# Performance work log

Hardware: AMD Instinct MI355X
Metric: run time of the kernel (lower is better)

The kernel has to match this reference:

```python
import jax, jax.numpy as jnp
import numpy as np

N = 100_000      # nodes
E = 1_600_000    # edges (avg degree 16)
FIN = 128
FOUT = 64
C = 1.0          # Poincare ball curvature (args.c)
T = 0.48         # threshold (forward default)
MIN_NORM = 1e-15
PROJ_EPS = 4e-3  # float32 boundary eps used by standard PoincareBall.proj


def _artanh(x):
    x = jnp.clip(x, -1.0 + 1e-7, 1.0 - 1e-7)
    return 0.5 * (jnp.log1p(x) - jnp.log1p(-x))


def logmap0(p, c):
    sc = c ** 0.5
    n = jnp.clip(jnp.linalg.norm(p, axis=-1, keepdims=True), MIN_NORM, None)
    return p / (sc * n) * _artanh(sc * n)


def expmap0(u, c):
    sc = c ** 0.5
    n = jnp.clip(jnp.linalg.norm(u, axis=-1, keepdims=True), MIN_NORM, None)
    return jnp.tanh(sc * n) * u / (sc * n)


def proj(x, c):
    n = jnp.clip(jnp.linalg.norm(x, axis=-1, keepdims=True), MIN_NORM, None)
    maxn = (1.0 - PROJ_EPS) / (c ** 0.5)
    return jnp.where(n > maxn, x / n * maxn, x)


def setup_inputs() -> dict:
    key = jax.random.key(0)
    k0, k1, k2, k3, k4 = jax.random.split(key, 5)
    # points near the origin of the Poincare ball
    x = jax.random.normal(k0, (N, FIN), dtype=jnp.float32) * 0.05
    edge_index = jax.random.randint(k1, (2, E), 0, N, dtype=jnp.int32)
    W_up = jax.random.normal(k2, (FIN, FOUT), dtype=jnp.float32) / np.float32(np.sqrt(FIN))
    W_pl = jax.random.normal(k3, (FOUT, 2), dtype=jnp.float32) / np.float32(np.sqrt(FOUT))
    W_lw = jax.random.normal(k4, (2 * FOUT, 1), dtype=jnp.float32) / np.float32(np.sqrt(2 * FOUT))
    return {"x": x, "edge_index": edge_index, "W_up": W_up, "W_pl": W_pl, "W_lw": W_lw}


def reference(x, edge_index, W_up, W_pl, W_lw):
    src, dst = edge_index[0], edge_index[1]

    def agg(v):  # PyG add-aggregation: out[i] = sum_{(j->i)} v[j]
        return jax.ops.segment_sum(v[src], dst, num_segments=N)

    x_tan = logmap0(x, C)                                   # [N, FIN]
    updated_x = jax.nn.leaky_relu(x_tan @ W_up)             # [N, FOUT], slope 0.01
    sum_neigh = agg(updated_x)                              # [N, FOUT]
    random_prob = jax.nn.softmax(jax.nn.relu(sum_neigh @ W_pl), axis=-1)  # [N, 2]
    sel_v = jnp.where(random_prob[:, 1:2] > T, 1.0, 0.0)    # [N, 1] hard gate
    sum_sel = agg(sel_v * updated_x)                        # [N, FOUT]
    weight_sel = jax.nn.sigmoid(jnp.concatenate([sum_sel, sum_neigh], axis=-1) @ W_lw)  # [N, 1]
    a_x = jax.nn.relu(agg(weight_sel * sel_v * updated_x))  # [N, FOUT]
    out = updated_x + a_x
    return proj(expmap0(out, C), C)
```

## Files before the change

kernel.cpp:

```cpp
#include <hip/hip_runtime.h>
#include <math.h>

#define FIN 128
#define FOUT 64
#define MAXDEG 64
#define BKT_SHIFT 7
#define BKT_CAP 2560


__device__ __forceinline__ float4 f4add(float4 a, float4 b) {
  return make_float4(a.x + b.x, a.y + b.y, a.z + b.z, a.w + b.w);
}
__device__ __forceinline__ float4 f4fma(float c, float4 v, float4 a) {
  return make_float4(fmaf(c, v.x, a.x), fmaf(c, v.y, a.y),
                     fmaf(c, v.z, a.z), fmaf(c, v.w, a.w));
}
__device__ __forceinline__ float4 f4shflxor(float4 v, int off) {
  return make_float4(__shfl_xor(v.x, off, 64), __shfl_xor(v.y, off, 64),
                     __shfl_xor(v.z, off, 64), __shfl_xor(v.w, off, 64));
}
__device__ __forceinline__ float red16(float v) {
  v += __shfl_xor(v, 1, 64);
  v += __shfl_xor(v, 2, 64);
  v += __shfl_xor(v, 4, 64);
  v += __shfl_xor(v, 8, 64);
  return v;
}

__device__ __forceinline__ float row_scale(float ss) {
  float n  = sqrtf(ss);
  float nc = fmaxf(n, 1e-15f);
  float t  = fminf(nc, 1.0f - 1e-7f);
  float at = 0.5f * (log1pf(t) - log1pf(-t));
  return at / nc;
}

__device__ __forceinline__ float leaky(float v) {
  return (v >= 0.f) ? v : 0.01f * v;
}

__device__ __forceinline__ unsigned int bf16rne(float x) {
  unsigned int b = __float_as_uint(x);
  b += 0x7FFFu + ((b >> 16) & 1u);
  return b >> 16;
}
__device__ __forceinline__ float4 bf4(uint2 v) {
  return make_float4(__uint_as_float(v.x << 16),
                     __uint_as_float(v.x & 0xFFFF0000u),
                     __uint_as_float(v.y << 16),
                     __uint_as_float(v.y & 0xFFFF0000u));
}

__global__ __launch_bounds__(256) void k_main(const float* __restrict__ x,
                                              const float* __restrict__ Wup,
                                              const float* __restrict__ Wpl,
                                              const float* __restrict__ Wlw,
                                              float* __restrict__ u,
                                              float* __restrict__ scl4,
                                              const int* __restrict__ ei, int E,
                                              int nb, int* __restrict__ bcnt,
                                              int2* __restrict__ stg,
                                              int N, int gemmBlocks) {
  __shared__ float buf[8192];
  __shared__ float wls[256];
  __shared__ float ps[256];
  __shared__ float scl[64];

  int t = threadIdx.x;

  if (blockIdx.x >= gemmBlocks) {
    int* hist = (int*)buf;
    int* base = hist + nb;
    int bb = blockIdx.x - gemmBlocks;
    for (int h = t; h < nb; h += 256) hist[h] = 0;
    __syncthreads();
    int e0 = bb * 4096 + t * 16;
    int sv[16], dv[16];
#pragma unroll
    for (int j = 0; j < 16; j += 4) {
      int e = e0 + j;
      if (e + 3 < E) {
        int4 s4 = *(const int4*)(ei + e);
        int4 d4 = *(const int4*)(ei + E + e);
        sv[j] = s4.x; sv[j+1] = s4.y; sv[j+2] = s4.z; sv[j+3] = s4.w;
        dv[j] = d4.x; dv[j+1] = d4.y; dv[j+2] = d4.z; dv[j+3] = d4.w;
      } else {
        for (int q = 0; q < 4; ++q) {
          int ee = e + q;
          sv[j+q] = (ee < E) ? ei[ee] : -1;
          dv[j+q] = (ee < E) ? ei[E + ee] : -1;
        }
      }
    }
#pragma unroll
    for (int j = 0; j < 16; ++j)
      if (dv[j] >= 0) atomicAdd(&hist[dv[j] >> BKT_SHIFT], 1);
    __syncthreads();
    for (int h = t; h < nb; h += 256)
      base[h] = hist[h] ? atomicAdd(&bcnt[h], hist[h]) : 0;
    __syncthreads();
    for (int h = t; h < nb; h += 256) hist[h] = 0;
    __syncthreads();
#pragma unroll
    for (int j = 0; j < 16; ++j) {
      if (dv[j] < 0) continue;
      int b = dv[j] >> BKT_SHIFT;
      int p = base[b] + atomicAdd(&hist[b], 1);
      if (p < BKT_CAP) stg[(size_t)b * BKT_CAP + p] = make_int2(sv[j], dv[j]);
    }
    return;
  }

  int n0 = blockIdx.x * 64;
  {
    int proj = t >> 6, f = t & 63;
    float wv = (proj == 0) ? Wpl[f * 2]
             : (proj == 1) ? Wpl[f * 2 + 1]
             : (proj == 2) ? Wlw[f] : Wlw[64 + f];
    wls[t] = wv;
  }

  {
    int n  = t & 63;
    int kq = t >> 6;
    int gn = n0 + n;
    bool ok = gn < N;
    const float4* xr = (const float4*)(x + (size_t)gn * FIN);
    float ssum = 0.f;
    float4 r0[8];
#pragma unroll
    for (int m = 0; m < 8; ++m)
      r0[m] = ok ? xr[kq * 8 + m] : make_float4(0.f, 0.f, 0.f, 0.f);
#pragma unroll
    for (int m = 0; m < 8; ++m) {
      float4 v = r0[m];
      ssum = fmaf(v.x, v.x, fmaf(v.y, v.y, fmaf(v.z, v.z, fmaf(v.w, v.w, ssum))));
      int kf = kq * 32 + m * 4;
      buf[(kf + 0) * 64 + n] = v.x;
      buf[(kf + 1) * 64 + n] = v.y;
      buf[(kf + 2) * 64 + n] = v.z;
      buf[(kf + 3) * 64 + n] = v.w;
    }
    ps[t] = ssum;
  }
  __syncthreads();
  if (t < 64) scl[t] = row_scale(ps[t] + ps[t + 64] + ps[t + 128] + ps[t + 192]);

  int wave = t >> 6, lane = t & 63;
  int j = lane & 3, i = lane >> 2;
  const float* xp = buf + i * 4;
  const float* wg = Wup + wave * 16 + j * 4;
  float4 a0 = make_float4(0,0,0,0), a1 = a0, a2 = a0, a3 = a0;
#pragma unroll 8
  for (int k = 0; k < FIN; ++k) {
    float4 xv = *(const float4*)(xp + k * 64);
    float4 wv = *(const float4*)(wg + k * 64);
    a0 = f4fma(xv.x, wv, a0);
    a1 = f4fma(xv.y, wv, a1);
    a2 = f4fma(xv.z, wv, a2);
    a3 = f4fma(xv.w, wv, a3);
  }
  __syncthreads();

  int fbase = wave * 16 + j * 4;
#pragma unroll
  for (int r = 0; r < 4; ++r) {
    float4 acc = (r == 0) ? a0 : (r == 1) ? a1 : (r == 2) ? a2 : a3;
    int nn = i * 4 + r;
    int gnn = n0 + nn;
    float sc = scl[nn];
    float4 o = make_float4(leaky(sc * acc.x), leaky(sc * acc.y),
                           leaky(sc * acc.z), leaky(sc * acc.w));
    if (gnn < N) *(float4*)(u + (size_t)gnn * FOUT + fbase) = o;
    buf[nn * 67 + fbase]     = o.x;
    buf[nn * 67 + fbase + 1] = o.y;
    buf[nn * 67 + fbase + 2] = o.z;
    buf[nn * 67 + fbase + 3] = o.w;
  }
  __syncthreads();

  {
    int proj = t >> 6;
    const float* wc = wls + proj * 64;
    int nn = t & 63;
    int gnn = n0 + nn;
    const float* ur = buf + nn * 67;
    float acc = 0.f;
#pragma unroll 8
    for (int f = 0; f < 64; ++f) acc = fmaf(ur[f], wc[f], acc);
    if (gnn < N) scl4[(size_t)gnn * 4 + proj] = acc;
  }
}

__global__ __launch_bounds__(256) void k_binB(const int2* __restrict__ stg,
                                              const int* __restrict__ bcnt,
                                              int N, int* __restrict__ deg,
                                              int* __restrict__ slots) {
  __shared__ int cur[128];
  int b = blockIdx.x, t = threadIdx.x;
  if (t < 128) cur[t] = 0;
  __syncthreads();
  int cnt = min(bcnt[b], BKT_CAP);
  int dbase = b << BKT_SHIFT;
  const int2* sp = stg + (size_t)b * BKT_CAP;
  for (int i = t; i < cnt; i += 256) {
    int2 e = sp[i];
    int p = atomicAdd(&cur[e.y - dbase], 1);
    if (p < MAXDEG) slots[(size_t)e.y * MAXDEG + p] = e.x;
  }
  __syncthreads();
  if (t < 128) {
    int dst = dbase + t;
    if (dst < N) {
      int c = min(cur[t], MAXDEG);
      deg[dst] = c;
      int cr = (c + 15) & ~15;
      for (int p = c; p < cr; ++p) slots[(size_t)dst * MAXDEG + p] = N;
    }
  }
}

__global__ __launch_bounds__(256) void k_aggA(const int* __restrict__ deg,
                                              const int* __restrict__ slots,
                                              const float4* __restrict__ scl4,
                                              float* __restrict__ selF,
                                              float* __restrict__ gq,
                                              float* __restrict__ tp, int N) {
  int wv = threadIdx.x >> 6, lane = threadIdx.x & 63;
  int g = lane >> 4, l16 = lane & 15;
  int i = blockIdx.x * 16 + wv * 4 + g;
  bool act = (i < N);
  int d = act ? deg[i] : 0;
  float ax = 0.f, ay = 0.f, aw = 0.f;
#pragma unroll
  for (int q = 0; q < 4; ++q) {
    int k = l16 + q * 16;
    if (k < d) {
      int s = slots[(size_t)i * MAXDEG + k];
      float4 gg = scl4[s];
      ax += gg.x; ay += gg.y; aw += gg.w;
    }
  }
  ax = red16(ax); ay = red16(ay); aw = red16(aw);
  if (act && l16 == 0) {
    float r0 = fmaxf(ax, 0.f), r1 = fmaxf(ay, 0.f);
    float m  = fmaxf(r0, r1);
    float e0 = expf(r0 - m), e1 = expf(r1 - m);
    float p  = e1 / (e0 + e1);
    float sel = (p > 0.48f) ? 1.f : 0.f;
    float4 own = scl4[i];
    selF[i] = sel;
    gq[i]   = sel * own.z;
    tp[i]   = aw;
  }
}

__global__ __launch_bounds__(256) void k_wgt(const int* __restrict__ deg,
                                             const int* __restrict__ slots,
                                             const float* __restrict__ gq,
                                             const float* __restrict__ tp,
                                             const float* __restrict__ selF,
                                             const float* __restrict__ u,
                                             unsigned int* __restrict__ uw,
                                             int N) {
  if (blockIdx.x == 0 && threadIdx.x < 32)
    uw[(size_t)N * 32 + threadIdx.x] = 0u;
  int wv = threadIdx.x >> 6, lane = threadIdx.x & 63;
  int g = lane >> 4, l16 = lane & 15;
  int i = blockIdx.x * 16 + wv * 4 + g;
  bool act = (i < N);
  int d = act ? deg[i] : 0;
  float a = 0.f;
#pragma unroll
  for (int q = 0; q < 4; ++q) {
    int k = l16 + q * 16;
    if (k < d) a += gq[slots[(size_t)i * MAXDEG + k]];
  }
  a = red16(a);
  if (!act) return;
  if (selF[i] != 0.f) {
    float sig = 1.f / (1.f + expf(-(tp[i] + a)));
    float4 uv = ((const float4*)(u + (size_t)i * 64))[l16];
    unsigned int b0 = bf16rne(sig * uv.x), b1 = bf16rne(sig * uv.y);
    unsigned int b2 = bf16rne(sig * uv.z), b3 = bf16rne(sig * uv.w);
    ((uint2*)(uw + (size_t)i * 32))[l16] =
        make_uint2(b0 | (b1 << 16), b2 | (b3 << 16));
  }
}

__global__ __launch_bounds__(256) void k_agg3(const int* __restrict__ deg,
                                              const int* __restrict__ slots,
                                              const float* __restrict__ selF,
                                              const float* __restrict__ u,
                                              const uint2* __restrict__ uw,
                                              float* __restrict__ out, int N) {
  __shared__ int comp[4][64];
  int wv = threadIdx.x >> 6, lane = threadIdx.x & 63;
  int i = blockIdx.x * 4 + wv;
  if (i >= N) return;
  int d = deg[i];
  bool valid = lane < d;
  int s = 0;
  if (valid) s = slots[(size_t)i * MAXDEG + lane];
  bool flag = valid && (selF[s] != 0.f);
  unsigned long long mask = __ballot(flag);
  int cnt = __popcll(mask);
  comp[wv][lane] = N;
  int rank = __popcll(mask & ((1ull << lane) - 1ull));
  if (flag) comp[wv][rank] = s;
  int sub = lane >> 4, l4 = lane & 15;
  float4 acc0 = make_float4(0, 0, 0, 0), acc1 = acc0;
  for (int k0 = 0; k0 < cnt; k0 += 8) {
    int s0 = comp[wv][k0 + sub];
    int s1 = comp[wv][k0 + sub + 4];
    uint2 w0 = uw[(size_t)s0 * 16 + l4];
    uint2 w1 = uw[(size_t)s1 * 16 + l4];
    acc0 = f4add(acc0, bf4(w0));
    acc1 = f4add(acc1, bf4(w1));
  }
  float4 acc = f4add(acc0, acc1);
  acc = f4add(acc, f4shflxor(acc, 16));
  acc = f4add(acc, f4shflxor(acc, 32));
  float4 uv = ((const float4*)(u + (size_t)i * 64))[l4];
  float4 ov = make_float4(uv.x + fmaxf(acc.x, 0.f), uv.y + fmaxf(acc.y, 0.f),
                          uv.z + fmaxf(acc.z, 0.f), uv.w + fmaxf(acc.w, 0.f));
  float ssp = ov.x * ov.x + ov.y * ov.y + ov.z * ov.z + ov.w * ov.w;
  float ss  = red16(ssp);
  float nc  = fmaxf(sqrtf(ss), 1e-15f);
  float th  = tanhf(nc);
  float fac = th / nc;
  float4 r = make_float4(ov.x * fac, ov.y * fac, ov.z * fac, ov.w * fac);
  float n2 = fmaxf(th, 1e-15f);
  float maxn = 1.0f - 4e-3f;
  float sc = (n2 > maxn) ? (maxn / n2) : 1.0f;
  float4 res = make_float4(r.x * sc, r.y * sc, r.z * sc, r.w * sc);
  if (sub == 0) ((float4*)(out + (size_t)i * 64))[l4] = res;
}

extern "C" void kernel_launch(void* const* d_in, const int* in_sizes, int n_in,
                              void* d_out, int out_size, void* d_ws, size_t ws_size,
                              hipStream_t stream) {
  const float* x   = (const float*)d_in[0];
  const int*   ei  = (const int*)d_in[1];
  const float* Wup = (const float*)d_in[2];
  const float* Wpl = (const float*)d_in[3];
  const float* Wlw = (const float*)d_in[4];
  float* out = (float*)d_out;

  int N = in_sizes[0] / FIN;
  int E = in_sizes[1] / 2;
  int nb = (N + (1 << BKT_SHIFT) - 1) >> BKT_SHIFT;

  char* ws = (char*)d_ws;
  float* u     = (float*)ws;
  int*   slots = (int*)(u + (size_t)N * 64);
  char*  regB  = (char*)(slots + (size_t)N * MAXDEG);
  size_t regB_sz = (size_t)nb * BKT_CAP * sizeof(int2);
  int2*  stg   = (int2*)regB;
  unsigned int* uwp = (unsigned int*)regB;
  float* scl4  = (float*)(regB + regB_sz);
  int*   deg   = (int*)(scl4 + (size_t)N * 4);
  float* selF  = (float*)(deg + N);
  float* gq    = selF + N;
  float* tp    = gq + N;
  int*   bcnt  = (int*)(tp + N);

  hipMemsetAsync(bcnt, 0, nb * sizeof(int), stream);

  int gemmBlocks = (N + 63) / 64;
  int binABlocks = (E + 4095) / 4096;
  k_main<<<gemmBlocks + binABlocks, 256, 0, stream>>>(
      x, Wup, Wpl, Wlw, u, scl4, ei, E, nb, bcnt, stg, N, gemmBlocks);
  k_binB<<<nb, 256, 0, stream>>>(stg, bcnt, N, deg, slots);
  int nblk16 = (N + 15) / 16;
  k_aggA<<<nblk16, 256, 0, stream>>>(deg, slots, (const float4*)scl4, selF, gq, tp, N);
  k_wgt<<<nblk16, 256, 0, stream>>>(deg, slots, gq, tp, selF, u, uwp, N);
  k_agg3<<<(N + 3) / 4, 256, 0, stream>>>(deg, slots, selF, u, (const uint2*)uwp, out, N);
}
```

Measured before the change: 220.8 us.

## Compact selected neighbor slots in k_wgt and use 16-lane-per-node final aggregation

k_wgt now reads a packed (sel, sel*z) pair per neighbor, ballots the selected neighbors, and rewrites each node's slot list in place so it holds only selected sources, plus a per-node count. k_agg3 then gathers over only the compacted selected list with 16 lanes per node and 16 nodes per block, with no shuffle reduction and no per-edge selection lookup. The binning buckets shrink to 64 destinations with a smaller capacity, and the padding writes in k_binB are dropped. This moves selection filtering earlier to cut redundant gathers and wave underuse in the final pass. The cost is that the smaller bucket capacity makes overflow truncation more likely if degrees cluster.

Result: faster. 211.6 us (-4.2%).

```diff
diff --git a/kernel.cpp b/kernel.cpp
--- a/kernel.cpp
+++ b/kernel.cpp
@@ -4,8 +4,8 @@
 #define FIN 128
 #define FOUT 64
 #define MAXDEG 64
-#define BKT_SHIFT 7
-#define BKT_CAP 2560
+#define BKT_SHIFT 6
+#define BKT_CAP 1376
 
 
 __device__ __forceinline__ float4 f4add(float4 a, float4 b) {
@@ -14,10 +14,6 @@
 __device__ __forceinline__ float4 f4fma(float c, float4 v, float4 a) {
   return make_float4(fmaf(c, v.x, a.x), fmaf(c, v.y, a.y),
                      fmaf(c, v.z, a.z), fmaf(c, v.w, a.w));
-}
-__device__ __forceinline__ float4 f4shflxor(float4 v, int off) {
-  return make_float4(__shfl_xor(v.x, off, 64), __shfl_xor(v.y, off, 64),
-                     __shfl_xor(v.z, off, 64), __shfl_xor(v.w, off, 64));
 }
 __device__ __forceinline__ float red16(float v) {
   v += __shfl_xor(v, 1, 64);
@@ -196,9 +192,9 @@
                                               const int* __restrict__ bcnt,
                                               int N, int* __restrict__ deg,
                                               int* __restrict__ slots) {
-  __shared__ int cur[128];
+  __shared__ int cur[64];
   int b = blockIdx.x, t = threadIdx.x;
-  if (t < 128) cur[t] = 0;
+  if (t < 64) cur[t] = 0;
   __syncthreads();
   int cnt = min(bcnt[b], BKT_CAP);
   int dbase = b << BKT_SHIFT;
@@ -209,22 +205,16 @@
     if (p < MAXDEG) slots[(size_t)e.y * MAXDEG + p] = e.x;
   }
   __syncthreads();
-  if (t < 128) {
+  if (t < 64) {
     int dst = dbase + t;
-    if (dst < N) {
-      int c = min(cur[t], MAXDEG);
-      deg[dst] = c;
-      int cr = (c + 15) & ~15;
-      for (int p = c; p < cr; ++p) slots[(size_t)dst * MAXDEG + p] = N;
-    }
+    if (dst < N) deg[dst] = min(cur[t], MAXDEG);
   }
 }
 
 __global__ __launch_bounds__(256) void k_aggA(const int* __restrict__ deg,
                                               const int* __restrict__ slots,
                                               const float4* __restrict__ scl4,
-                                              float* __restrict__ selF,
-                                              float* __restrict__ gq,
+                                              float2* __restrict__ gs,
                                               float* __restrict__ tp, int N) {
   int wv = threadIdx.x >> 6, lane = threadIdx.x & 63;
   int g = lane >> 4, l16 = lane & 15;
@@ -249,20 +239,18 @@
     float p  = e1 / (e0 + e1);
     float sel = (p > 0.48f) ? 1.f : 0.f;
     float4 own = scl4[i];
-    selF[i] = sel;
-    gq[i]   = sel * own.z;
-    tp[i]   = aw;
+    gs[i] = make_float2(sel, sel * own.z);
+    tp[i] = aw;
   }
 }
 
 __global__ __launch_bounds__(256) void k_wgt(const int* __restrict__ deg,
-                                             const int* __restrict__ slots,
-                                             const float* __restrict__ gq,
+                                             int* __restrict__ slots,
+                                             const float2* __restrict__ gs,
                                              const float* __restrict__ tp,
-                                             const float* __restrict__ selF,
                                              const float* __restrict__ u,
                                              unsigned int* __restrict__ uw,
-                                             int N) {
+                                             int* __restrict__ scnt, int N) {
   if (blockIdx.x == 0 && threadIdx.x < 32)
     uw[(size_t)N * 32 + threadIdx.x] = 0u;
   int wv = threadIdx.x >> 6, lane = threadIdx.x & 63;
@@ -270,15 +258,43 @@
   int i = blockIdx.x * 16 + wv * 4 + g;
   bool act = (i < N);
   int d = act ? deg[i] : 0;
+  int sv[4]; bool f[4];
   float a = 0.f;
 #pragma unroll
   for (int q = 0; q < 4; ++q) {
     int k = l16 + q * 16;
-    if (k < d) a += gq[slots[(size_t)i * MAXDEG + k]];
+    bool valid = k < d;
+    int s = 0;
+    if (valid) s = slots[(size_t)i * MAXDEG + k];
+    sv[q] = s;
+    float2 gv = make_float2(0.f, 0.f);
+    if (valid) gv = gs[s];
+    f[q] = valid && (gv.x != 0.f);
+    a += gv.y;
   }
   a = red16(a);
+  unsigned long long m0 = __ballot(f[0]);
+  unsigned long long m1 = __ballot(f[1]);
+  unsigned long long m2 = __ballot(f[2]);
+  unsigned long long m3 = __ballot(f[3]);
+  int sh = g * 16;
+  unsigned gm0 = (unsigned)(m0 >> sh) & 0xFFFFu;
+  unsigned gm1 = (unsigned)(m1 >> sh) & 0xFFFFu;
+  unsigned gm2 = (unsigned)(m2 >> sh) & 0xFFFFu;
+  unsigned gm3 = (unsigned)(m3 >> sh) & 0xFFFFu;
+  int c0 = __popc(gm0), c1 = __popc(gm1), c2 = __popc(gm2);
+  unsigned lm = (1u << l16) - 1u;
+  int r0 = __popc(gm0 & lm);
+  int r1 = c0 + __popc(gm1 & lm);
+  int r2 = c0 + c1 + __popc(gm2 & lm);
+  int r3 = c0 + c1 + c2 + __popc(gm3 & lm);
   if (!act) return;
-  if (selF[i] != 0.f) {
+  if (f[0]) slots[(size_t)i * MAXDEG + r0] = sv[0];
+  if (f[1]) slots[(size_t)i * MAXDEG + r1] = sv[1];
+  if (f[2]) slots[(size_t)i * MAXDEG + r2] = sv[2];
+  if (f[3]) slots[(size_t)i * MAXDEG + r3] = sv[3];
+  if (l16 == 0) scnt[i] = c0 + c1 + c2 + __popc(gm3);
+  if (gs[i].x != 0.f) {
     float sig = 1.f / (1.f + expf(-(tp[i] + a)));
     float4 uv = ((const float4*)(u + (size_t)i * 64))[l16];
     unsigned int b0 = bf16rne(sig * uv.x), b1 = bf16rne(sig * uv.y);
@@ -288,40 +304,34 @@
   }
 }
 
-__global__ __launch_bounds__(256) void k_agg3(const int* __restrict__ deg,
+__global__ __launch_bounds__(256) void k_agg3(const int* __restrict__ scnt,
                                               const int* __restrict__ slots,
-                                              const float* __restrict__ selF,
+                                              const uint2* __restrict__ uw,
                                               const float* __restrict__ u,
-                                              const uint2* __restrict__ uw,
                                               float* __restrict__ out, int N) {
-  __shared__ int comp[4][64];
+  __shared__ int comp[16][64];
   int wv = threadIdx.x >> 6, lane = threadIdx.x & 63;
-  int i = blockIdx.x * 4 + wv;
-  if (i >= N) return;
-  int d = deg[i];
-  bool valid = lane < d;
-  int s = 0;
-  if (valid) s = slots[(size_t)i * MAXDEG + lane];
-  bool flag = valid && (selF[s] != 0.f);
-  unsigned long long mask = __ballot(flag);
-  int cnt = __popcll(mask);
-  comp[wv][lane] = N;
-  int rank = __popcll(mask & ((1ull << lane) - 1ull));
-  if (flag) comp[wv][rank] = s;
-  int sub = lane >> 4, l4 = lane & 15;
-  float4 acc0 = make_float4(0, 0, 0, 0), acc1 = acc0;
-  for (int k0 = 0; k0 < cnt; k0 += 8) {
-    int s0 = comp[wv][k0 + sub];
-    int s1 = comp[wv][k0 + sub + 4];
-    uint2 w0 = uw[(size_t)s0 * 16 + l4];
-    uint2 w1 = uw[(size_t)s1 * 16 + l4];
-    acc0 = f4add(acc0, bf4(w0));
-    acc1 = f4add(acc1, bf4(w1));
-  }
-  float4 acc = f4add(acc0, acc1);
-  acc = f4add(acc, f4shflxor(acc, 16));
-  acc = f4add(acc, f4shflxor(acc, 32));
-  float4 uv = ((const float4*)(u + (size_t)i * 64))[l4];
+  int g = lane >> 4, l16 = lane & 15;
+  int nloc = wv * 4 + g;
+  int i = blockIdx.x * 16 + nloc;
+  bool act = (i < N);
+  int sc = act ? scnt[i] : 0;
+#pragma unroll
+  for (int b = 0; b < 4; ++b) {
+    int idx = b * 16 + l16;
+    comp[nloc][idx] = (idx < sc) ? slots[(size_t)i * MAXDEG + idx] : N;
+  }
+  float4 acc = make_float4(0.f, 0.f, 0.f, 0.f);
+  for (int r = 0; r < sc; r += 4) {
+#pragma unroll
+    for (int j = 0; j < 4; ++j) {
+      int s = (r + j < sc) ? comp[nloc][r + j] : N;
+      uint2 w = uw[(size_t)s * 16 + l16];
+      acc = f4add(acc, bf4(w));
+    }
+  }
+  if (!act) return;
+  float4 uv = ((const float4*)(u + (size_t)i * 64))[l16];
   float4 ov = make_float4(uv.x + fmaxf(acc.x, 0.f), uv.y + fmaxf(acc.y, 0.f),
                           uv.z + fmaxf(acc.z, 0.f), uv.w + fmaxf(acc.w, 0.f));
   float ssp = ov.x * ov.x + ov.y * ov.y + ov.z * ov.z + ov.w * ov.w;
@@ -332,9 +342,9 @@
   float4 r = make_float4(ov.x * fac, ov.y * fac, ov.z * fac, ov.w * fac);
   float n2 = fmaxf(th, 1e-15f);
   float maxn = 1.0f - 4e-3f;
-  float sc = (n2 > maxn) ? (maxn / n2) : 1.0f;
-  float4 res = make_float4(r.x * sc, r.y * sc, r.z * sc, r.w * sc);
-  if (sub == 0) ((float4*)(out + (size_t)i * 64))[l4] = res;
+  float sc2 = (n2 > maxn) ? (maxn / n2) : 1.0f;
+  float4 res = make_float4(r.x * sc2, r.y * sc2, r.z * sc2, r.w * sc2);
+  ((float4*)(out + (size_t)i * 64))[l16] = res;
 }
 
 extern "C" void kernel_launch(void* const* d_in, const int* in_sizes, int n_in,
@@ -360,10 +370,10 @@
   unsigned int* uwp = (unsigned int*)regB;
   float* scl4  = (float*)(regB + regB_sz);
   int*   deg   = (int*)(scl4 + (size_t)N * 4);
-  float* selF  = (float*)(deg + N);
-  float* gq    = selF + N;
-  float* tp    = gq + N;
-  int*   bcnt  = (int*)(tp + N);
+  float2* gs   = (float2*)(deg + N);
+  float* tp    = (float*)(gs + N);
+  int*   scnt  = (int*)(tp + N);
+  int*   bcnt  = scnt + N;
 
   hipMemsetAsync(bcnt, 0, nb * sizeof(int), stream);
 
@@ -373,7 +383,7 @@
       x, Wup, Wpl, Wlw, u, scl4, ei, E, nb, bcnt, stg, N, gemmBlocks);
   k_binB<<<nb, 256, 0, stream>>>(stg, bcnt, N, deg, slots);
   int nblk16 = (N + 15) / 16;
-  k_aggA<<<nblk16, 256, 0, stream>>>(deg, slots, (const float4*)scl4, selF, gq, tp, N);
-  k_wgt<<<nblk16, 256, 0, stream>>>(deg, slots, gq, tp, selF, u, uwp, N);
-  k_agg3<<<(N + 3) / 4, 256, 0, stream>>>(deg, slots, selF, u, (const uint2*)uwp, out, N);
-}
+  k_aggA<<<nblk16, 256, 0, stream>>>(deg, slots, (const float4*)scl4, gs, tp, N);
+  k_wgt<<<nblk16, 256, 0, stream>>>(deg, slots, (const float2*)gs, tp, u, uwp, scnt, N);
+  k_agg3<<<nblk16, 256, 0, stream>>>(scnt, slots, (const uint2*)uwp, u, out, N);
+}
```
